# Performance work log

Measured on AMD Instinct MI355X. Metric: run time of the kernel, lower is better.

## Reference

```python
import jax, jax.numpy as jnp
import numpy as np

NUM_HEADS = 12


def setup_inputs() -> dict:
    key = jax.random.key(0)
    ks = jax.random.split(key, 5)
    B, S, D = 4, 2048, 768
    scale = 0.02
    return {
        "hidden_states": jax.random.normal(ks[0], (B, S, D), dtype=jnp.float32),
        "c_attn_w": jax.random.normal(ks[1], (D, 3 * D), dtype=jnp.float32) * scale,
        "c_attn_b": jax.random.normal(ks[2], (3 * D,), dtype=jnp.float32) * scale,
        "c_proj_w": jax.random.normal(ks[3], (D, D), dtype=jnp.float32) * scale,
        "c_proj_b": jax.random.normal(ks[4], (D,), dtype=jnp.float32) * scale,
    }


def reference(hidden_states, c_attn_w, c_attn_b, c_proj_w, c_proj_b):
    B, S, D = hidden_states.shape
    H = NUM_HEADS
    hd = D // H

    # fused QKV projection (HF Conv1D: x @ W + b, W is [in, out])
    qkv = hidden_states @ c_attn_w + c_attn_b  # [B, S, 3D]
    q, k, v = jnp.split(qkv, 3, axis=-1)

    def split_heads(t):
        return t.reshape(B, S, H, hd).transpose(0, 2, 1, 3)  # [B, H, S, hd]

    q, k, v = split_heads(q), split_heads(k), split_heads(v)

    # scaled dot-product scores (scale_attn_weights=True -> / sqrt(head_dim))
    scores = jnp.einsum("bhqd,bhkd->bhqk", q, k) / jnp.asarray(
        np.sqrt(hd), dtype=q.dtype
    )

    # causal mask: where(tril, scores, dtype_min) as in eager GPT2Attention
    causal = jnp.tril(jnp.ones((S, S), dtype=bool))
    mask_value = jnp.finfo(scores.dtype).min
    scores = jnp.where(causal[None, None, :, :], scores, mask_value)

    attn = jax.nn.softmax(scores, axis=-1)  # attn_dropout p=0 (eval)

    out = jnp.einsum("bhqk,bhkd->bhqd", attn, v)
    out = out.transpose(0, 2, 1, 3).reshape(B, S, D)  # merge heads

    # output projection (resid_dropout p=0)
    return out @ c_proj_w + c_proj_b
```

## Files before the change

kernel.cpp:

```cpp
#include <hip/hip_runtime.h>
#include <stdint.h>

typedef __attribute__((ext_vector_type(8))) short short8;
typedef __attribute__((ext_vector_type(4))) short short4v;
typedef __attribute__((ext_vector_type(8))) __bf16 bf16x8;
typedef __attribute__((ext_vector_type(4))) float f32x4;

#define SEQ 2048
#define DMODEL 768
#define NHEAD 12
#define HD 64
#define NBATCH 4

__device__ __forceinline__ float bf2f(unsigned short u) {
    return __uint_as_float(((unsigned int)u) << 16);
}
__device__ __forceinline__ unsigned short f2bf(float f) {
    unsigned int u = __float_as_uint(f);
    u += 0x7fffu + ((u >> 16) & 1u);
    return (unsigned short)(u >> 16);
}
__device__ __forceinline__ unsigned short f2bfn(float f) {
    union { __bf16 h; unsigned short u; } cv;
    cv.h = (__bf16)f;
    return cv.u;
}
__device__ __forceinline__ short8 cvt8(float4 a, float4 b) {
    short8 r;
    r[0] = (short)f2bf(a.x); r[1] = (short)f2bf(a.y);
    r[2] = (short)f2bf(a.z); r[3] = (short)f2bf(a.w);
    r[4] = (short)f2bf(b.x); r[5] = (short)f2bf(b.y);
    r[6] = (short)f2bf(b.z); r[7] = (short)f2bf(b.w);
    return r;
}
__device__ __forceinline__ f32x4 mfma16(short8 a, short8 b, f32x4 c) {
    return __builtin_amdgcn_mfma_f32_16x16x32_bf16(
        __builtin_bit_cast(bf16x8, a), __builtin_bit_cast(bf16x8, b), c, 0, 0, 0);
}
__device__ __forceinline__ f32x4 mfma16k16(short4v a, short4v b, f32x4 c) {
#if __has_builtin(__builtin_amdgcn_mfma_f32_16x16x16bf16_1k)
    return __builtin_amdgcn_mfma_f32_16x16x16bf16_1k(a, b, c, 0, 0, 0);
#else
    asm("v_mfma_f32_16x16x16_bf16 %0, %1, %2, %0" : "+v"(c) : "v"(a), "v"(b));
    return c;
#endif
}
__device__ __forceinline__ void gload16(const unsigned short* g, unsigned short* l) {
    __builtin_amdgcn_global_load_lds(
        (const __attribute__((address_space(1))) unsigned int*)g,
        (__attribute__((address_space(3))) unsigned int*)l, 16, 0, 0);
}

__global__ void detect_k(const unsigned short* x, const unsigned short* w1,
                         const unsigned short* b1, const unsigned short* w2,
                         const unsigned short* b2, int* flags) {
    const int w = threadIdx.x >> 6, l = threadIdx.x & 63;
    if (w >= 5) return;
    const unsigned short* ptrs[5] = {x, w1, b1, w2, b2};
    const unsigned short* p = ptrs[w];
    float mx = 0.f;
    for (int j = l; j < 1024; j += 64) {
        float v = fabsf(bf2f(p[j]));
        if (!(v <= 1e30f)) v = 1e31f;
        if (v > mx) mx = v;
    }
#pragma unroll
    for (int off = 1; off < 64; off <<= 1) mx = fmaxf(mx, __shfl_xor(mx, off, 64));
    if (l == 0) flags[w] = (mx > 1e3f) ? 1 : 0;
}

__global__ __launch_bounds__(256) void cvt_x(
    const float* __restrict__ Xf, const unsigned short* __restrict__ Xh,
    unsigned short* __restrict__ Xb, const int* __restrict__ flags, int n8) {
    int i = blockIdx.x * 256 + threadIdx.x;
    if (i >= n8) return;
    if (flags[0]) {
        float4 a = ((const float4*)Xf)[(size_t)i * 2];
        float4 b = ((const float4*)Xf)[(size_t)i * 2 + 1];
        *(short8*)&Xb[(size_t)i * 8] = cvt8(a, b);
    } else {
        ((uint4*)Xb)[i] = ((const uint4*)Xh)[i];
    }
}

__global__ __launch_bounds__(256) void convert_wt(
    const float* __restrict__ Wf, const unsigned short* __restrict__ Wh,
    unsigned short* __restrict__ Wt, int R, int C,
    const int* __restrict__ flags, int fidx) {

    __shared__ unsigned short tile[64][65];
    const int c0 = blockIdx.x * 64, r0 = blockIdx.y * 64;
    const int t = threadIdx.x;
    const int ri = t >> 2, cj = (t & 3) * 16;
    const bool f32 = flags[fidx] != 0;

    if (f32) {
#pragma unroll
        for (int u = 0; u < 4; u++) {
            float4 v = *(const float4*)&Wf[(size_t)(r0 + ri) * C + c0 + cj + u * 4];
            tile[ri][cj + u * 4 + 0] = f2bf(v.x);
            tile[ri][cj + u * 4 + 1] = f2bf(v.y);
            tile[ri][cj + u * 4 + 2] = f2bf(v.z);
            tile[ri][cj + u * 4 + 3] = f2bf(v.w);
        }
    } else {
        uint4 a = *(const uint4*)&Wh[(size_t)(r0 + ri) * C + c0 + cj];
        uint4 b = *(const uint4*)&Wh[(size_t)(r0 + ri) * C + c0 + cj + 8];
        *(uint4*)&tile[ri][cj] = a;
        *(uint4*)&tile[ri][cj + 8] = b;
    }
    __syncthreads();

    const int ci = t >> 2, rj = (t & 3) * 16;
    unsigned short tmp[16];
#pragma unroll
    for (int u = 0; u < 16; u++) tmp[u] = tile[rj + u][ci];
    *(uint4*)&Wt[(size_t)(c0 + ci) * R + r0 + rj]     = *(uint4*)&tmp[0];
    *(uint4*)&Wt[(size_t)(c0 + ci) * R + r0 + rj + 8] = *(uint4*)&tmp[8];
}

__global__ __launch_bounds__(256, 3) void gemm_bt(
    const float* __restrict__ Af, const unsigned short* __restrict__ Ah,
    const unsigned short* __restrict__ Bt,
    const float* __restrict__ biasf, const unsigned short* __restrict__ biash,
    int K, int mode, const int* __restrict__ flags, int aFidx, int bFidx,
    unsigned short* __restrict__ out0, unsigned short* __restrict__ out1,
    unsigned short* __restrict__ out2, float* __restrict__ outf) {

    __shared__ __align__(16) unsigned short As[128][32];
    __shared__ __align__(16) unsigned short Bs[128][32];

    int bx = blockIdx.x, by = blockIdx.y;
    {
        const int nwg = (int)(gridDim.x * gridDim.y);
        if ((nwg & 7) == 0) {
            int bid = by * gridDim.x + bx;
            const int cpx = nwg >> 3;
            bid = (bid & 7) * cpx + (bid >> 3);
            bx = bid % gridDim.x;
            by = bid / gridDim.x;
        }
    }
    const int mBase = by * 128;
    const int nBase = bx * 128;
    const int t = threadIdx.x;
    const int w = t >> 6, l = t & 63, lr = l & 15, lk = l >> 4;
    const int wr = w >> 1, wc = w & 1;

    const bool af32 = (aFidx >= 0) && (flags[aFidx] != 0);
    const bool bf32 = flags[bFidx] != 0;

    f32x4 zero = {0.f, 0.f, 0.f, 0.f};
    f32x4 acc[4][4];
#pragma unroll
    for (int i = 0; i < 4; i++)
#pragma unroll
        for (int j = 0; j < 4; j++) acc[i][j] = zero;

    const int arow = t >> 2;
    const int acol = (t & 3) * 8;
    const float* Afp = Af + (size_t)mBase * K;
    const unsigned short* Ahp = Ah + (size_t)mBase * K;
    const unsigned short* Bp = Bt + (size_t)nBase * K;

    const int ch0 = (w * 2 + 0) * 64 + l;
    const int ch1 = (w * 2 + 1) * 64 + l;
    unsigned short* BsF = &Bs[0][0];
    unsigned short* AsF = &As[0][0];

    for (int k0 = 0; k0 < K; k0 += 32) {
        gload16(&Bp[(size_t)(ch0 >> 2) * K + k0 + (ch0 & 3) * 8], BsF + (size_t)(w * 2 + 0) * 512);
        gload16(&Bp[(size_t)(ch1 >> 2) * K + k0 + (ch1 & 3) * 8], BsF + (size_t)(w * 2 + 1) * 512);
        if (af32) {
            float4 f0 = *(const float4*)&Afp[(size_t)arow * K + k0 + acol];
            float4 f1 = *(const float4*)&Afp[(size_t)arow * K + k0 + acol + 4];
            float4 f2 = *(const float4*)&Afp[(size_t)(arow + 64) * K + k0 + acol];
            float4 f3 = *(const float4*)&Afp[(size_t)(arow + 64) * K + k0 + acol + 4];
            *(short8*)&As[arow][acol]      = cvt8(f0, f1);
            *(short8*)&As[arow + 64][acol] = cvt8(f2, f3);
        } else {
            gload16(&Ahp[(size_t)(ch0 >> 2) * K + k0 + (ch0 & 3) * 8], AsF + (size_t)(w * 2 + 0) * 512);
            gload16(&Ahp[(size_t)(ch1 >> 2) * K + k0 + (ch1 & 3) * 8], AsF + (size_t)(w * 2 + 1) * 512);
        }
        __syncthreads();

        short8 a[4], b[4];
#pragma unroll
        for (int i = 0; i < 4; i++)
            a[i] = *(const short8*)&As[wr * 64 + i * 16 + lr][lk * 8];
#pragma unroll
        for (int j = 0; j < 4; j++)
            b[j] = *(const short8*)&Bs[wc * 64 + j * 16 + lr][lk * 8];
#pragma unroll
        for (int i = 0; i < 4; i++)
#pragma unroll
            for (int j = 0; j < 4; j++) acc[i][j] = mfma16(a[i], b[j], acc[i][j]);
        __syncthreads();
    }

#pragma unroll
    for (int j = 0; j < 4; j++) {
        int col = nBase + wc * 64 + j * 16 + lr;
        float bv = bf32 ? biasf[col] : bf2f(biash[col]);
        if (mode == 0 && col >= 1536) {
            int c2 = col - 1536;
            int h = c2 >> 6, d = c2 & 63;
#pragma unroll
            for (int i = 0; i < 4; i++) {
                int row0 = mBase + wr * 64 + i * 16 + lk * 4;
                int bb = row0 >> 11, s0 = row0 & 2047;
                short4v hv4;
#pragma unroll
                for (int r = 0; r < 4; r++) hv4[r] = (short)f2bf(acc[i][j][r] + bv);
                *(short4v*)&out2[(((size_t)(bb * NHEAD + h)) * HD + d) * SEQ + s0] = hv4;
            }
        } else {
#pragma unroll
            for (int i = 0; i < 4; i++) {
                int row0 = mBase + wr * 64 + i * 16 + lk * 4;
#pragma unroll
                for (int r = 0; r < 4; r++) {
                    int row = row0 + r;
                    float fv = acc[i][j][r] + bv;
                    if (mode == 0) {
                        int bb = row >> 11;
                        int s  = row & 2047;
                        unsigned short hv = f2bf(fv);
                        if (col < 768) {
                            int h = col >> 6, d = col & 63;
                            out0[(((size_t)(bb * NHEAD + h)) * SEQ + s) * HD + d] = hv;
                        } else {
                            int c2 = col - 768;
                            int h = c2 >> 6, d = c2 & 63;
                            out1[(((size_t)(bb * NHEAD + h)) * SEQ + s) * HD + d] = hv;
                        }
                    } else {
                        outf[(size_t)row * DMODEL + col] = fv;
                    }
                }
            }
        }
    }
}

__global__ __launch_bounds__(256, 3) void flash_attn(
    const unsigned short* __restrict__ Q, const unsigned short* __restrict__ Km,
    const unsigned short* __restrict__ Vt, unsigned short* __restrict__ Oatt) {

    const int h  = blockIdx.x;
    const int px = blockIdx.y;
    const int b  = blockIdx.z;
    const int bh = b * NHEAD + h;
    const int qtA = 31 - px;
    const int qtB = px;
    const int t = threadIdx.x, w = t >> 6, l = t & 63, lr = l & 15, lk = l >> 4;
    const int qbA = qtA * 64 + w * 16;
    const int qbB = qtB * 64 + w * 16;

    const unsigned short* Qp = Q + (size_t)bh * SEQ * HD;
    const unsigned short* Kp = Km + (size_t)bh * SEQ * HD;
    const unsigned short* Vp = Vt + (size_t)bh * HD * SEQ;

    __shared__ __align__(16) unsigned short Ks[2][4096];
    __shared__ __align__(16) unsigned short Vs[2][4096];

    short8 qA0 = *(const short8*)&Qp[(size_t)(qbA + lr) * HD + lk * 8];
    short8 qA1 = *(const short8*)&Qp[(size_t)(qbA + lr) * HD + 32 + lk * 8];
    short8 qB0 = *(const short8*)&Qp[(size_t)(qbB + lr) * HD + lk * 8];
    short8 qB1 = *(const short8*)&Qp[(size_t)(qbB + lr) * HD + 32 + lk * 8];

    f32x4 zero = {0.f, 0.f, 0.f, 0.f};
    f32x4 oA[4], oB[4];
    float lsumA = 0.f, lsumB = 0.f;
#pragma unroll
    for (int dt = 0; dt < 4; dt++) { oA[dt] = zero; oB[dt] = zero; }

    const float SCL2E = 0.125f * 1.44269504088896f;

#pragma unroll
    for (int q = 0; q < 2; ++q) {
        const int c = w * 128 + q * 64 + l;
        const int row = c >> 3;
        const int ch = (c & 7) ^ (row & 7);
        gload16(&Kp[(size_t)row * HD + ch * 8], &Ks[0][(w * 128 + q * 64) * 8]);
        gload16(&Vp[(size_t)row * SEQ + ch * 8], &Vs[0][(w * 128 + q * 64) * 8]);
    }
    __syncthreads();

    for (int kt = 0; kt <= qtA; ++kt) {
        const int cur = kt & 1;
        if (kt < qtA) {
            const int kn = kt + 1;
#pragma unroll
            for (int q = 0; q < 2; ++q) {
                const int c = w * 128 + q * 64 + l;
                const int row = c >> 3;
                const int ch = (c & 7) ^ (row & 7);
                gload16(&Kp[(size_t)(kn * 64 + row) * HD + ch * 8],
                        &Ks[cur ^ 1][(w * 128 + q * 64) * 8]);
                gload16(&Vp[(size_t)row * SEQ + kn * 64 + ch * 8],
                        &Vs[cur ^ 1][(w * 128 + q * 64) * 8]);
            }
        }
        const bool doB = (kt <= qtB);

        f32x4 s0[4], s1[4];
#pragma unroll
        for (int ct = 0; ct < 4; ct++) { s0[ct] = zero; s1[ct] = zero; }
#pragma unroll
        for (int ct = 0; ct < 4; ct++) {
            const int row = ct * 16 + lr, sw = row & 7;
            short8 k0 = *(const short8*)&Ks[cur][(row * 8 + (lk ^ sw)) * 8];
            short8 k1 = *(const short8*)&Ks[cur][(row * 8 + ((4 | lk) ^ sw)) * 8];
            s0[ct] = mfma16(k0, qA0, s0[ct]);
            s0[ct] = mfma16(k1, qA1, s0[ct]);
            if (doB) {
                s1[ct] = mfma16(k0, qB0, s1[ct]);
                s1[ct] = mfma16(k1, qB1, s1[ct]);
            }
        }

        short4v vf[4][4];
#pragma unroll
        for (int dt = 0; dt < 4; dt++) {
            const int row = dt * 16 + lr;
            const int sw = row & 7;
#pragma unroll
            for (int ct = 0; ct < 4; ct++) {
                const int g = 2 * ct + (lk >> 1);
                const int hh = lk & 1;
                vf[dt][ct] = *(const short4v*)&Vs[cur][(row * 8 + (g ^ sw)) * 8 + hh * 4];
            }
        }

        short4v paA[4];
        {
            float p[4][4];
#pragma unroll
            for (int ct = 0; ct < 4; ct++)
#pragma unroll
                for (int r = 0; r < 4; r++) p[ct][r] = s0[ct][r] * SCL2E;
            if (kt == qtA) {
                const int qrow = qbA + lr;
#pragma unroll
                for (int ct = 0; ct < 4; ct++) {
#pragma unroll
                    for (int r = 0; r < 4; r++) {
                        const int key = kt * 64 + ct * 16 + lk * 4 + r;
                        if (key > qrow) p[ct][r] = -30000.0f;
                    }
                }
            }
#pragma unroll
            for (int ct = 0; ct < 4; ct++)
#pragma unroll
                for (int r = 0; r < 4; r++) p[ct][r] = exp2f(p[ct][r]);
#pragma unroll
            for (int ct = 0; ct < 4; ct++)
                lsumA += (p[ct][0] + p[ct][1]) + (p[ct][2] + p[ct][3]);
#pragma unroll
            for (int ct = 0; ct < 4; ct++) {
                short4v pk;
#pragma unroll
                for (int r = 0; r < 4; r++) pk[r] = (short)f2bfn(p[ct][r]);
                paA[ct] = pk;
            }
        }
#pragma unroll
        for (int dt = 0; dt < 4; dt++)
#pragma unroll
            for (int ct = 0; ct < 4; ct++)
                oA[dt] = mfma16k16(paA[ct], vf[dt][ct], oA[dt]);

        if (doB) {
            short4v paB[4];
            float p[4][4];
#pragma unroll
            for (int ct = 0; ct < 4; ct++)
#pragma unroll
                for (int r = 0; r < 4; r++) p[ct][r] = s1[ct][r] * SCL2E;
            if (kt == qtB) {
                const int qrow = qbB + lr;
#pragma unroll
                for (int ct = 0; ct < 4; ct++) {
#pragma unroll
                    for (int r = 0; r < 4; r++) {
                        const int key = kt * 64 + ct * 16 + lk * 4 + r;
                        if (key > qrow) p[ct][r] = -30000.0f;
                    }
                }
            }
#pragma unroll
            for (int ct = 0; ct < 4; ct++)
#pragma unroll
                for (int r = 0; r < 4; r++) p[ct][r] = exp2f(p[ct][r]);
#pragma unroll
            for (int ct = 0; ct < 4; ct++)
                lsumB += (p[ct][0] + p[ct][1]) + (p[ct][2] + p[ct][3]);
#pragma unroll
            for (int ct = 0; ct < 4; ct++) {
                short4v pk;
#pragma unroll
                for (int r = 0; r < 4; r++) pk[r] = (short)f2bfn(p[ct][r]);
                paB[ct] = pk;
            }
#pragma unroll
            for (int dt = 0; dt < 4; dt++)
#pragma unroll
                for (int ct = 0; ct < 4; ct++)
                    oB[dt] = mfma16k16(paB[ct], vf[dt][ct], oB[dt]);
        }

        __syncthreads();
    }

    lsumA += __shfl_xor(lsumA, 16, 64);
    lsumA += __shfl_xor(lsumA, 32, 64);
    lsumB += __shfl_xor(lsumB, 16, 64);
    lsumB += __shfl_xor(lsumB, 32, 64);

#pragma unroll
    for (int r = 0; r < 4; r++) {
        const float invA = 1.0f / __shfl(lsumA, lk * 4 + r, 64);
        const float invB = 1.0f / __shfl(lsumB, lk * 4 + r, 64);
        const int rowA = qbA + lk * 4 + r;
        const int rowB = qbB + lk * 4 + r;
#pragma unroll
        for (int dt = 0; dt < 4; dt++) {
            Oatt[((size_t)(b * SEQ) + rowA) * DMODEL + h * HD + dt * 16 + lr] =
                f2bfn(oA[dt][r] * invA);
            Oatt[((size_t)(b * SEQ) + rowB) * DMODEL + h * HD + dt * 16 + lr] =
                f2bfn(oB[dt][r] * invB);
        }
    }
}

extern "C" void kernel_launch(void* const* d_in, const int* in_sizes, int n_in,
                              void* d_out, int out_size, void* d_ws, size_t ws_size,
                              hipStream_t stream) {
    const void *X = d_in[0], *W1 = d_in[1], *b1 = d_in[2], *W2 = d_in[3], *b2 = d_in[4];
    for (int i = 0; i < n_in; i++) {
        switch (in_sizes[i]) {
            case NBATCH * SEQ * DMODEL: X  = d_in[i]; break;
            case DMODEL * 3 * DMODEL:   W1 = d_in[i]; break;
            case 3 * DMODEL:            b1 = d_in[i]; break;
            case DMODEL * DMODEL:       W2 = d_in[i]; break;
            case DMODEL:                b2 = d_in[i]; break;
        }
    }
    float* out = (float*)d_out;

    int* flags = (int*)d_ws;
    unsigned short* base = (unsigned short*)d_ws + 64;
    unsigned short* Wt1 = base;
    unsigned short* Wt2 = Wt1 + (size_t)2304 * 768;

    const size_t headElems = (size_t)NHEAD * SEQ * HD;
    const size_t xElems = (size_t)NBATCH * SEQ * DMODEL;
    const size_t fixedElems = 64 + (size_t)2304 * 768 + (size_t)768 * 768;
    const size_t mergedNeed = (fixedElems + xElems + 4 * NBATCH * headElems) * 2 + 1024;
    const bool merged = ws_size >= mergedNeed;

    detect_k<<<1, 320, 0, stream>>>(
        (const unsigned short*)X, (const unsigned short*)W1,
        (const unsigned short*)b1, (const unsigned short*)W2,
        (const unsigned short*)b2, flags);

    convert_wt<<<dim3(2304 / 64, 768 / 64), 256, 0, stream>>>(
        (const float*)W1, (const unsigned short*)W1, Wt1, 768, 2304, flags, 1);
    convert_wt<<<dim3(768 / 64, 768 / 64), 256, 0, stream>>>(
        (const float*)W2, (const unsigned short*)W2, Wt2, 768, 768, flags, 3);

    if (merged) {
        unsigned short* Xb  = Wt2 + (size_t)768 * 768;
        unsigned short* Qw  = Xb + xElems;
        unsigned short* Kw  = Qw + (size_t)NBATCH * headElems;
        unsigned short* Vtw = Kw + (size_t)NBATCH * headElems;
        unsigned short* Aw  = Vtw + (size_t)NBATCH * headElems;

        cvt_x<<<(int)((xElems / 8 + 255) / 256), 256, 0, stream>>>(
            (const float*)X, (const unsigned short*)X, Xb, flags, (int)(xElems / 8));

        gemm_bt<<<dim3(2304 / 128, NBATCH * SEQ / 128), 256, 0, stream>>>(
            nullptr, Xb, Wt1,
            (const float*)b1, (const unsigned short*)b1,
            DMODEL, 0, flags, -1, 2, Qw, Kw, Vtw, nullptr);

        flash_attn<<<dim3(NHEAD, 16, NBATCH), 256, 0, stream>>>(Qw, Kw, Vtw, Aw);

        gemm_bt<<<dim3(768 / 128, NBATCH * SEQ / 128), 256, 0, stream>>>(
            nullptr, Aw, Wt2,
            (const float*)b2, (const unsigned short*)b2,
            DMODEL, 1, flags, -1, 4, nullptr, nullptr, nullptr, out);
    } else {
        unsigned short* Qw  = Wt2 + (size_t)768 * 768;
        unsigned short* Kw  = Qw + headElems;
        unsigned short* Vtw = Kw + headElems;
        unsigned short* Aw  = Vtw + headElems;
        for (int batch = 0; batch < NBATCH; ++batch) {
            const size_t xoff = (size_t)batch * SEQ * DMODEL;

            gemm_bt<<<dim3(2304 / 128, SEQ / 128), 256, 0, stream>>>(
                (const float*)X + xoff, (const unsigned short*)X + xoff, Wt1,
                (const float*)b1, (const unsigned short*)b1,
                DMODEL, 0, flags, 0, 2, Qw, Kw, Vtw, nullptr);

            flash_attn<<<dim3(NHEAD, 16, 1), 256, 0, stream>>>(Qw, Kw, Vtw, Aw);

            gemm_bt<<<dim3(768 / 128, SEQ / 128), 256, 0, stream>>>(
                nullptr, Aw, Wt2,
                (const float*)b2, (const unsigned short*)b2,
                DMODEL, 1, flags, -1, 4, nullptr, nullptr, nullptr, out + xoff);
        }
    }
}
```

Baseline: 241.8 us.

## Load K/V fragments directly from global memory, drop LDS staging and barriers

The flash attention kernel no longer stages K and V tiles through double-buffered shared memory with async global-to-LDS copies. Each wave now reads its MFMA operand fragments straight from global memory, relying on L1/L2 to serve the 4x redundant reads across waves, and the per-iteration __syncthreads is removed. The B-side QK MFMAs are moved after the A softmax, the PV MFMAs for both tiles are grouped at the end, and s_setprio raises wave priority around the MFMA blocks. The risk is higher global and cache traffic and exposed load latency, since nothing is prefetched a tile ahead.

```diff
diff --git a/kernel.cpp b/kernel.cpp
--- a/kernel.cpp
+++ b/kernel.cpp
@@ -261,9 +261,6 @@
     const unsigned short* Kp = Km + (size_t)bh * SEQ * HD;
     const unsigned short* Vp = Vt + (size_t)bh * HD * SEQ;
 
-    __shared__ __align__(16) unsigned short Ks[2][4096];
-    __shared__ __align__(16) unsigned short Vs[2][4096];
-
     short8 qA0 = *(const short8*)&Qp[(size_t)(qbA + lr) * HD + lk * 8];
     short8 qA1 = *(const short8*)&Qp[(size_t)(qbA + lr) * HD + 32 + lk * 8];
     short8 qB0 = *(const short8*)&Qp[(size_t)(qbB + lr) * HD + lk * 8];
@@ -277,61 +274,39 @@
 
     const float SCL2E = 0.125f * 1.44269504088896f;
 
-#pragma unroll
-    for (int q = 0; q < 2; ++q) {
-        const int c = w * 128 + q * 64 + l;
-        const int row = c >> 3;
-        const int ch = (c & 7) ^ (row & 7);
-        gload16(&Kp[(size_t)row * HD + ch * 8], &Ks[0][(w * 128 + q * 64) * 8]);
-        gload16(&Vp[(size_t)row * SEQ + ch * 8], &Vs[0][(w * 128 + q * 64) * 8]);
-    }
-    __syncthreads();
+    const unsigned short* Kfb = Kp + (size_t)lr * HD + lk * 8;
+    const unsigned short* Vfb = Vp + (size_t)lr * SEQ + lk * 4;
 
     for (int kt = 0; kt <= qtA; ++kt) {
-        const int cur = kt & 1;
-        if (kt < qtA) {
-            const int kn = kt + 1;
-#pragma unroll
-            for (int q = 0; q < 2; ++q) {
-                const int c = w * 128 + q * 64 + l;
-                const int row = c >> 3;
-                const int ch = (c & 7) ^ (row & 7);
-                gload16(&Kp[(size_t)(kn * 64 + row) * HD + ch * 8],
-                        &Ks[cur ^ 1][(w * 128 + q * 64) * 8]);
-                gload16(&Vp[(size_t)row * SEQ + kn * 64 + ch * 8],
-                        &Vs[cur ^ 1][(w * 128 + q * 64) * 8]);
-            }
-        }
         const bool doB = (kt <= qtB);
-
-        f32x4 s0[4], s1[4];
-#pragma unroll
-        for (int ct = 0; ct < 4; ct++) { s0[ct] = zero; s1[ct] = zero; }
+        const unsigned short* Kt = Kfb + (size_t)kt * 64 * HD;
+
+        short8 kf0[4], kf1[4];
 #pragma unroll
         for (int ct = 0; ct < 4; ct++) {
-            const int row = ct * 16 + lr, sw = row & 7;
-            short8 k0 = *(const short8*)&Ks[cur][(row * 8 + (lk ^ sw)) * 8];
-            short8 k1 = *(const short8*)&Ks[cur][(row * 8 + ((4 | lk) ^ sw)) * 8];
-            s0[ct] = mfma16(k0, qA0, s0[ct]);
-            s0[ct] = mfma16(k1, qA1, s0[ct]);
-            if (doB) {
-                s1[ct] = mfma16(k0, qB0, s1[ct]);
-                s1[ct] = mfma16(k1, qB1, s1[ct]);
-            }
+            kf0[ct] = *(const short8*)&Kt[(size_t)ct * 16 * HD];
+            kf1[ct] = *(const short8*)&Kt[(size_t)ct * 16 * HD + 32];
         }
 
         short4v vf[4][4];
 #pragma unroll
         for (int dt = 0; dt < 4; dt++) {
-            const int row = dt * 16 + lr;
-            const int sw = row & 7;
-#pragma unroll
-            for (int ct = 0; ct < 4; ct++) {
-                const int g = 2 * ct + (lk >> 1);
-                const int hh = lk & 1;
-                vf[dt][ct] = *(const short4v*)&Vs[cur][(row * 8 + (g ^ sw)) * 8 + hh * 4];
-            }
-        }
+            const unsigned short* Vr = Vfb + (size_t)dt * 16 * SEQ + kt * 64;
+#pragma unroll
+            for (int ct = 0; ct < 4; ct++)
+                vf[dt][ct] = *(const short4v*)&Vr[ct * 16];
+        }
+
+        f32x4 s0[4];
+#pragma unroll
+        for (int ct = 0; ct < 4; ct++) s0[ct] = zero;
+        __builtin_amdgcn_s_setprio(1);
+#pragma unroll
+        for (int ct = 0; ct < 4; ct++) {
+            s0[ct] = mfma16(kf0[ct], qA0, s0[ct]);
+            s0[ct] = mfma16(kf1[ct], qA1, s0[ct]);
+        }
+        __builtin_amdgcn_s_setprio(0);
 
         short4v paA[4];
         {
@@ -343,13 +318,12 @@
             if (kt == qtA) {
                 const int qrow = qbA + lr;
 #pragma unroll
-                for (int ct = 0; ct < 4; ct++) {
+                for (int ct = 0; ct < 4; ct++)
 #pragma unroll
                     for (int r = 0; r < 4; r++) {
                         const int key = kt * 64 + ct * 16 + lk * 4 + r;
                         if (key > qrow) p[ct][r] = -30000.0f;
                     }
-                }
             }
 #pragma unroll
             for (int ct = 0; ct < 4; ct++)
@@ -366,14 +340,19 @@
                 paA[ct] = pk;
             }
         }
-#pragma unroll
-        for (int dt = 0; dt < 4; dt++)
-#pragma unroll
-            for (int ct = 0; ct < 4; ct++)
-                oA[dt] = mfma16k16(paA[ct], vf[dt][ct], oA[dt]);
-
+
+        short4v paB[4];
         if (doB) {
-            short4v paB[4];
+            f32x4 s1[4];
+#pragma unroll
+            for (int ct = 0; ct < 4; ct++) s1[ct] = zero;
+            __builtin_amdgcn_s_setprio(1);
+#pragma unroll
+            for (int ct = 0; ct < 4; ct++) {
+                s1[ct] = mfma16(kf0[ct], qB0, s1[ct]);
+                s1[ct] = mfma16(kf1[ct], qB1, s1[ct]);
+            }
+            __builtin_amdgcn_s_setprio(0);
             float p[4][4];
 #pragma unroll
             for (int ct = 0; ct < 4; ct++)
@@ -382,13 +361,12 @@
             if (kt == qtB) {
                 const int qrow = qbB + lr;
 #pragma unroll
-                for (int ct = 0; ct < 4; ct++) {
+                for (int ct = 0; ct < 4; ct++)
 #pragma unroll
                     for (int r = 0; r < 4; r++) {
                         const int key = kt * 64 + ct * 16 + lk * 4 + r;
                         if (key > qrow) p[ct][r] = -30000.0f;
                     }
-                }
             }
 #pragma unroll
             for (int ct = 0; ct < 4; ct++)
@@ -404,14 +382,22 @@
                 for (int r = 0; r < 4; r++) pk[r] = (short)f2bfn(p[ct][r]);
                 paB[ct] = pk;
             }
+        }
+
+        __builtin_amdgcn_s_setprio(1);
+#pragma unroll
+        for (int dt = 0; dt < 4; dt++)
+#pragma unroll
+            for (int ct = 0; ct < 4; ct++)
+                oA[dt] = mfma16k16(paA[ct], vf[dt][ct], oA[dt]);
+        if (doB) {
 #pragma unroll
             for (int dt = 0; dt < 4; dt++)
 #pragma unroll
                 for (int ct = 0; ct < 4; ct++)
                     oB[dt] = mfma16k16(paB[ct], vf[dt][ct], oB[dt]);
         }
-
-        __syncthreads();
+        __builtin_amdgcn_s_setprio(0);
     }
 
     lsumA += __shfl_xor(lsumA, 16, 64);
```

Result: slower. 387.2 us (+60.2%).
